# Kernel optimization log

Measured on AMD Instinct MI355X. Metric: run time of the kernel, lower is better.

The kernel has to match this reference:

```python
import jax, jax.numpy as jnp
import numpy as np
from functools import partial

H = 512
V = 32000


def setup_inputs() -> dict:
    key = jax.random.key(0)
    ks = jax.random.split(key, 16)
    B, Td, Te = 16, 64, 64
    s = 0.02
    inp = {
        'input_seqs': jax.random.normal(ks[0], (B, Td, H), jnp.float32),
        'input_lengths': jax.random.randint(ks[1], (B,), 1, Td + 1, jnp.int32),
        'encoder_outputs': jax.random.normal(ks[2], (B, Te, H), jnp.float32),
        'encoder_length': jax.random.randint(ks[3], (B,), 1, Te + 1, jnp.int32),
        # GRU (1 layer, batch_first): PyTorch layout W_ih (3H,H), W_hh (3H,H)
        'W_ih': jax.random.normal(ks[4], (3 * H, H), jnp.float32) * s,
        'W_hh': jax.random.normal(ks[5], (3 * H, H), jnp.float32) * s,
        'b_ih': jnp.zeros((3 * H,), jnp.float32),
        'b_hh': jnp.zeros((3 * H,), jnp.float32),
        # Attn: W: Linear(2H -> H), v: Linear(H -> 1)
        'W_attn': jax.random.normal(ks[6], (H, 2 * H), jnp.float32) * s,
        'b_attn': jnp.zeros((H,), jnp.float32),
        'v_w': jax.random.normal(ks[7], (H,), jnp.float32) * s,
        'v_b': jnp.zeros((), jnp.float32),
        # dense: Linear(2H -> H), output: Linear(H -> V)
        'W_dense': jax.random.normal(ks[8], (H, 2 * H), jnp.float32) * s,
        'b_dense': jnp.zeros((H,), jnp.float32),
        'W_out': jax.random.normal(ks[9], (V, H), jnp.float32) * s,
        'b_out': jnp.zeros((V,), jnp.float32),
    }
    return inp


def gru_forward(x, lengths, W_ih, W_hh, b_ih, b_hh):
    # Emulates pack_padded_sequence + GRU + pad_packed_sequence:
    # hidden state frozen past each sequence's length, outputs zero there.
    B, T, Hd = x.shape
    x_proj = jnp.einsum('bth,gh->btg', x, W_ih) + b_ih  # (B,T,3H)

    def step(h, inp):
        xp, t = inp  # xp: (B,3H)
        hp = h @ W_hh.T + b_hh
        xr, xz, xn = jnp.split(xp, 3, axis=-1)
        hr, hz, hn = jnp.split(hp, 3, axis=-1)
        r = jax.nn.sigmoid(xr + hr)
        z = jax.nn.sigmoid(xz + hz)
        n = jnp.tanh(xn + r * hn)
        h_new = (1.0 - z) * n + z * h
        valid = (t < lengths)[:, None]
        h_keep = jnp.where(valid, h_new, h)
        y = jnp.where(valid, h_new, 0.0)
        return h_keep, y

    h0 = jnp.zeros((B, Hd), x.dtype)
    h_last, ys = jax.lax.scan(step, h0, (x_proj.swapaxes(0, 1), jnp.arange(T)))
    return ys.swapaxes(0, 1), h_last  # (B,T,H), (B,H)


def attn_forward(enc, dec, enc_len, dec_len, W_attn, b_attn, v_w, v_b):
    B, Te, Hd = enc.shape
    Td = dec.shape[1]
    e_mask = (jnp.arange(Te) < enc_len[:, None])  # (B,Te)
    d_mask = (jnp.arange(Td) < dec_len[:, None])  # (B,Td)
    mask = (d_mask[:, :, None] & e_mask[:, None, :]).astype(enc.dtype)  # (B,Td,Te)
    # split W on the concat axis: cat(enc,dec) @ W.T = enc@We.T + dec@Wd.T
    We, Wd = W_attn[:, :Hd], W_attn[:, Hd:]
    enc_p = jnp.einsum('beh,gh->beg', enc, We)  # (B,Te,H)
    dec_p = jnp.einsum('bdh,gh->bdg', dec, Wd)  # (B,Td,H)
    m4 = mask[..., None]
    # masked-then-projected, matching enc_outputs*mask / dec_outputs*mask in torch
    score = jnp.tanh(enc_p[:, None, :, :] * m4 + dec_p[:, :, None, :] * m4 + b_attn)  # (B,Td,Te,H)
    energy = jnp.einsum('bdeh,h->bde', score, v_w) + v_b  # (B,Td,Te)
    a = jax.nn.softmax(energy, axis=2)  # softmax over ALL Te incl. masked (faithful)
    a_m = a * mask
    s = a_m.sum(axis=2)
    s = jnp.where(s == 0, 1.0, s)
    attention = a_m / s[:, :, None]  # (B,Td,Te)
    # attention is already zero where mask==0, so enc*mask == plain enc here
    context = jnp.einsum('bde,beh->bdh', attention, enc)
    return context  # dropout is identity at eval


def reference(input_seqs, input_lengths, encoder_outputs, encoder_length,
              W_ih, W_hh, b_ih, b_hh, W_attn, b_attn, v_w, v_b,
              W_dense, b_dense, W_out, b_out):
    dec_out, h_last = gru_forward(input_seqs, input_lengths, W_ih, W_hh, b_ih, b_hh)
    context = attn_forward(encoder_outputs, dec_out, encoder_length, input_lengths,
                           W_attn, b_attn, v_w, v_b)
    outputs = jnp.concatenate((dec_out, context), axis=2)  # (B,Td,2H)
    dense = jnp.tanh(jnp.einsum('bdg,hg->bdh', outputs, W_dense) + b_dense)
    logits = jnp.einsum('bdh,vh->bdv', dense, W_out) + b_out  # (B,Td,V)
    return logits, h_last[None]  # hidden: (n_layers=1, B, H)
```

## Files before the change

### kernel.cpp

```cpp
#include <hip/hip_runtime.h>
#include <stdint.h>


#define Hdim 512
#define Vdim 32000
#define Bdim 16
#define Tdim 64
#define BT   1024
#define GANG_BLOCKS 16
#define CVT_BLOCKS 64

typedef __attribute__((ext_vector_type(8))) short bf16x8;
typedef __attribute__((ext_vector_type(4))) float f32x4;

static __device__ __forceinline__ unsigned short f2bf(float f) {
    unsigned u = __float_as_uint(f);
    u = u + 0x7FFFu + ((u >> 16) & 1u);
    return (unsigned short)(u >> 16);
}
static __device__ __forceinline__ float bf2f(unsigned short h) {
    return __uint_as_float((unsigned)h << 16);
}
static __device__ __forceinline__ float fast_tanh(float x) {
    return 2.f / (1.f + __expf(-2.f * x)) - 1.f;
}


#define U_ZERO 8320
#define U_INP  131072
#define U_WIH  196608
#define U_WAT  131072
#define U_WDE  131072
#define U_ENC  131072
#define U_SPLIT (U_INP + U_WIH + U_WAT + U_WDE + U_ENC)
#define U_TOT  (U_ZERO + U_SPLIT)

__global__ __launch_bounds__(256) void preproc_kernel(
    const float* __restrict__ input_seqs,
    const float* __restrict__ W_ih,
    const float* __restrict__ W_attn,
    const float* __restrict__ W_dense,
    const float* __restrict__ enc,
    float* __restrict__ zero_base,
    unsigned short* __restrict__ inp_h, unsigned short* __restrict__ inp_l,
    unsigned short* __restrict__ Wih_h, unsigned short* __restrict__ Wih_l,
    unsigned short* __restrict__ Wat_h, unsigned short* __restrict__ Wat_l,
    unsigned short* __restrict__ Wde_h, unsigned short* __restrict__ Wde_l,
    unsigned short* __restrict__ enc_h, unsigned short* __restrict__ enc_l)
{
    int u = blockIdx.x * 256 + threadIdx.x;
    const int stride = gridDim.x * 256;
    for (; u < U_TOT; u += stride) {
        int r = u;
        if (r < U_ZERO) {
            float4 z; z.x = 0.f; z.y = 0.f; z.z = 0.f; z.w = 0.f;
            *(float4*)(zero_base + r * 4) = z;
            continue;
        }
        r -= U_ZERO;
        const float* src; unsigned short* hi; unsigned short* lo;
        if (r < U_INP) { src = input_seqs; hi = inp_h; lo = inp_l; }
        else { r -= U_INP;
            if (r < U_WIH) { src = W_ih; hi = Wih_h; lo = Wih_l; }
            else { r -= U_WIH;
                if (r < U_WAT) { src = W_attn; hi = Wat_h; lo = Wat_l; }
                else { r -= U_WAT;
                    if (r < U_WDE) { src = W_dense; hi = Wde_h; lo = Wde_l; }
                    else { r -= U_WDE; src = enc; hi = enc_h; lo = enc_l; }
                }
            }
        }
        int i = r * 4;
        float4 v = *(const float4*)(src + i);
        float f[4] = {v.x, v.y, v.z, v.w};
        unsigned short h[4], l[4];
#pragma unroll
        for (int k = 0; k < 4; ++k) {
            h[k] = f2bf(f[k]);
            l[k] = f2bf(f[k] - bf2f(h[k]));
        }
        *(uint2*)(hi + i) = *(const uint2*)h;
        *(uint2*)(lo + i) = *(const uint2*)l;
    }
}


struct GemmSmem {
    unsigned short AsH[128 * 40];
    unsigned short AsL[128 * 40];
    unsigned short BsH[128 * 40];
    unsigned short BsL[128 * 40];
};

static __device__ __forceinline__ void gemm_tile(
    GemmSmem& S, int m0, int n0,
    const unsigned short* __restrict__ Ah, const unsigned short* __restrict__ Al, int lda,
    const unsigned short* __restrict__ Bh, const unsigned short* __restrict__ Bl, int ldb,
    const float* __restrict__ bias,
    float* __restrict__ C, unsigned short* __restrict__ Cb, int ldc,
    int K, int act)
{
    const int tid = threadIdx.x;
    const int wave = tid >> 6, lane = tid & 63;
    const int wm = (wave >> 1) * 64, wn = (wave & 1) * 64;
    const int lrow = lane & 15, lk = (lane >> 4) * 8;

    f32x4 acc[4][4];
#pragma unroll
    for (int i = 0; i < 4; ++i)
#pragma unroll
        for (int j = 0; j < 4; ++j) acc[i][j] = (f32x4){0.f, 0.f, 0.f, 0.f};

    for (int k0 = 0; k0 < K; k0 += 32) {
#pragma unroll
        for (int i = 0; i < 2; ++i) {
            int idx = tid + i * 256;
            int rr = idx >> 2, kq = (idx & 3) * 8;
            size_t ao = (size_t)(m0 + rr) * lda + k0 + kq;
            size_t bo = (size_t)(n0 + rr) * ldb + k0 + kq;
            *(uint4*)(&S.AsH[rr * 40 + kq]) = *(const uint4*)(Ah + ao);
            *(uint4*)(&S.AsL[rr * 40 + kq]) = *(const uint4*)(Al + ao);
            *(uint4*)(&S.BsH[rr * 40 + kq]) = *(const uint4*)(Bh + bo);
            *(uint4*)(&S.BsL[rr * 40 + kq]) = *(const uint4*)(Bl + bo);
        }
        __syncthreads();
        bf16x8 ah[4], al[4], bh[4], bl[4];
#pragma unroll
        for (int i = 0; i < 4; ++i) {
            ah[i] = *(const bf16x8*)(&S.AsH[(wm + i * 16 + lrow) * 40 + lk]);
            al[i] = *(const bf16x8*)(&S.AsL[(wm + i * 16 + lrow) * 40 + lk]);
        }
#pragma unroll
        for (int j = 0; j < 4; ++j) {
            bh[j] = *(const bf16x8*)(&S.BsH[(wn + j * 16 + lrow) * 40 + lk]);
            bl[j] = *(const bf16x8*)(&S.BsL[(wn + j * 16 + lrow) * 40 + lk]);
        }
#pragma unroll
        for (int i = 0; i < 4; ++i)
#pragma unroll
            for (int j = 0; j < 4; ++j) {
                acc[i][j] = __builtin_amdgcn_mfma_f32_16x16x32_bf16(ah[i], bh[j], acc[i][j], 0, 0, 0);
                acc[i][j] = __builtin_amdgcn_mfma_f32_16x16x32_bf16(ah[i], bl[j], acc[i][j], 0, 0, 0);
                acc[i][j] = __builtin_amdgcn_mfma_f32_16x16x32_bf16(al[i], bh[j], acc[i][j], 0, 0, 0);
            }
        __syncthreads();
    }

    const int crow = m0 + wm + ((lane >> 4) * 4);
    const int ccol = n0 + wn + (lane & 15);
#pragma unroll
    for (int i = 0; i < 4; ++i) {
#pragma unroll
        for (int j = 0; j < 4; ++j) {
            int col = ccol + j * 16;
            float bv = bias[col];
#pragma unroll
            for (int rr = 0; rr < 4; ++rr) {
                int row = crow + i * 16 + rr;
                float v = acc[i][j][rr] + bv;
                if (act == 1) v = fast_tanh(v);
                if (Cb) Cb[(size_t)row * ldc + col] = f2bf(v);
                else    C [(size_t)row * ldc + col] = v;
            }
        }
    }
}

__global__ __launch_bounds__(256) void gemm_split(
    const unsigned short* __restrict__ Ah, const unsigned short* __restrict__ Al, int lda,
    const unsigned short* __restrict__ Bh, const unsigned short* __restrict__ Bl, int ldb,
    const float* __restrict__ bias,
    float* __restrict__ C, unsigned short* __restrict__ Cb, int ldc,
    int K, int act)
{
    __shared__ GemmSmem S;
    gemm_tile(S, blockIdx.y * 128, blockIdx.x * 128,
              Ah, Al, lda, Bh, Bl, ldb, bias, C, Cb, ldc, K, act);
}

__global__ __launch_bounds__(256) void gemm_split_dual(
    const unsigned short* __restrict__ A0h, const unsigned short* __restrict__ A0l,
    const unsigned short* __restrict__ B0h, const unsigned short* __restrict__ B0l,
    const float* __restrict__ bias0, float* __restrict__ C0,
    const unsigned short* __restrict__ A1h, const unsigned short* __restrict__ A1l,
    const unsigned short* __restrict__ B1h, const unsigned short* __restrict__ B1l,
    const float* __restrict__ bias1, float* __restrict__ C1)
{
    __shared__ GemmSmem S;
    const int bid = blockIdx.x;
    if (bid < 96) {
        gemm_tile(S, (bid / 12) * 128, (bid % 12) * 128,
                  A0h, A0l, Hdim, B0h, B0l, Hdim, bias0, C0, nullptr, 1536, Hdim, 0);
    } else {
        int r = bid - 96;
        gemm_tile(S, (r / 4) * 128, (r % 4) * 128,
                  A1h, A1l, Hdim, B1h, B1l, 1024, bias1, C1, nullptr, Hdim, Hdim, 0);
    }
}


__global__ __launch_bounds__(512) void gru_fused(
    const float* __restrict__ xp,
    const float* __restrict__ Whh,
    const float* __restrict__ bhh,
    const int*   __restrict__ lengths,
    unsigned long long* __restrict__ hslots,
    unsigned short* __restrict__ cath,
    unsigned short* __restrict__ catl,
    float* __restrict__ h_last,
    const float* __restrict__ Wout_f,
    unsigned short* __restrict__ Wout_bf)
{
    const int bid  = blockIdx.x;
    const int tid  = threadIdx.x;

    if (bid >= Bdim * GANG_BLOCKS) {
        int u = (bid - Bdim * GANG_BLOCKS) * 512 + tid;
        const int STR = CVT_BLOCKS * 512;
        for (; u < (Vdim * Hdim) / 4; u += STR) {
            float4 v = *(const float4*)(Wout_f + (size_t)u * 4);
            unsigned short h[4] = {f2bf(v.x), f2bf(v.y), f2bf(v.z), f2bf(v.w)};
            *(uint2*)(Wout_bf + (size_t)u * 4) = *(const uint2*)h;
        }
        return;
    }

    const int b    = bid >> 4;
    const int blk  = bid & 15;
    const int wave = tid >> 6, lane = tid & 63;
    const int j0 = blk * 32 + wave * 4;
    const int k0 = lane * 8;

    __shared__ float hl[2][512];
    __shared__ unsigned short yh_buf[64][32];
    __shared__ unsigned short yl_buf[64][32];

    float w[12][8];
#pragma unroll
    for (int g = 0; g < 3; ++g)
#pragma unroll
        for (int jj = 0; jj < 4; ++jj) {
            const float* src = Whh + (size_t)(g * 512 + j0 + jj) * Hdim + k0;
            float4 a = *(const float4*)src;
            float4 bq = *(const float4*)(src + 4);
            int r = g * 4 + jj;
            w[r][0] = a.x;  w[r][1] = a.y;  w[r][2] = a.z;  w[r][3] = a.w;
            w[r][4] = bq.x; w[r][5] = bq.y; w[r][6] = bq.z; w[r][7] = bq.w;
        }

    const int j = j0 + (lane & 3);
    float bh_r = 0.f, bh_z = 0.f, bh_n = 0.f;
    if (lane < 4) {
        bh_r = bhh[j]; bh_z = bhh[512 + j]; bh_n = bhh[1024 + j];
    }
    const int len_b = lengths[b];
    float hprev = 0.f;

    const size_t PSTR = (size_t)Bdim * Hdim;
    unsigned long long* gslot = hslots + (size_t)b * Hdim;
    const float* xbase = xp + (size_t)b * Tdim * 1536;

    for (int t = 0; t < Tdim; ++t) {
        const int par = t & 1;

        float xr = 0.f, xz = 0.f, xn = 0.f;
        if (lane < 4) {
            const float* xrow = xbase + (size_t)t * 1536;
            xr = xrow[j]; xz = xrow[512 + j]; xn = xrow[1024 + j];
        }

        if (wave == 0) {
            const unsigned long long* sl = gslot + (size_t)par * PSTR + k0;
            unsigned long long v[8];
            bool ok;
            do {
#pragma unroll
                for (int q = 0; q < 8; ++q)
                    v[q] = __hip_atomic_load(sl + q, __ATOMIC_RELAXED,
                                             __HIP_MEMORY_SCOPE_AGENT);
                ok = true;
#pragma unroll
                for (int q = 0; q < 8; ++q)
                    ok = ok && ((unsigned)(v[q] >> 32) == (unsigned)t);
            } while (!ok);
#pragma unroll
            for (int q = 0; q < 8; ++q)
                hl[par][q * 64 + lane] = __uint_as_float((unsigned)v[q]);
        }
        __syncthreads();

        float hv[8];
#pragma unroll
        for (int q = 0; q < 8; ++q) hv[q] = hl[par][q * 64 + lane];

        float p[12];
#pragma unroll
        for (int r = 0; r < 12; ++r) {
            float s = 0.f;
#pragma unroll
            for (int k = 0; k < 8; ++k) s += w[r][k] * hv[k];
            p[r] = s;
        }

#pragma unroll
        for (int off = 1; off < 64; off <<= 1)
#pragma unroll
            for (int r = 0; r < 12; ++r)
                p[r] += __shfl_xor(p[r], off);

        if (lane < 4) {
            const int jj = lane;
            float hr = p[jj]     + bh_r;
            float hz = p[4 + jj] + bh_z;
            float hn = p[8 + jj] + bh_n;
            float rg = 1.f / (1.f + __expf(-(xr + hr)));
            float zg = 1.f / (1.f + __expf(-(xz + hz)));
            float ng = fast_tanh(xn + rg * hn);
            float hnew = (1.f - zg) * ng + zg * hprev;
            bool valid = t < len_b;
            float hkeep = valid ? hnew : hprev;
            hprev = hkeep;
            if (t < Tdim - 1) {
                unsigned long long pv =
                    ((unsigned long long)(unsigned)(t + 1) << 32) |
                    (unsigned long long)__float_as_uint(hkeep);
                __hip_atomic_store(gslot + (size_t)((t + 1) & 1) * PSTR + j, pv,
                                   __ATOMIC_RELAXED, __HIP_MEMORY_SCOPE_AGENT);
            } else {
                h_last[b * Hdim + j] = hkeep;
            }
            float y = valid ? hnew : 0.f;
            unsigned short yh = f2bf(y);
            yh_buf[t][wave * 4 + jj] = yh;
            yl_buf[t][wave * 4 + jj] = f2bf(y - bf2f(yh));
        }
    }

    __syncthreads();
    for (int idx = tid; idx < 64 * 16; idx += 512) {
        int t = idx >> 4, c = (idx & 15) * 2;
        size_t off = (size_t)(b * Tdim + t) * 1024 + blk * 32 + c;
        *(unsigned*)(cath + off) = *(const unsigned*)(&yh_buf[t][c]);
        *(unsigned*)(catl + off) = *(const unsigned*)(&yl_buf[t][c]);
    }
}


__global__ __launch_bounds__(256) void attn_kernel(
    const float* __restrict__ encp,
    const float* __restrict__ decp,
    const float* __restrict__ enc,
    const float* __restrict__ battn,
    const float* __restrict__ vw,
    const float* __restrict__ vb,
    const int* __restrict__ enc_len,
    const int* __restrict__ dec_len,
    unsigned short* __restrict__ cath,
    unsigned short* __restrict__ catl)
{
    const int blk = blockIdx.x;
    const int b = blk >> 6, d = blk & 63;
    const int tid = threadIdx.x;
    const size_t obase = (size_t)(b * Tdim + d) * 1024 + 512;

    if (d >= dec_len[b]) {
        for (int h = tid; h < Hdim; h += 256) { cath[obase + h] = 0; catl[obase + h] = 0; }
        return;
    }
    const int Tv = enc_len[b];

    __shared__ float dpb[512];
    __shared__ float vwl[512];
    __shared__ float part[64][4];
    __shared__ float a_lds[64];

    if (tid < 128) {
        const float4* dp4 = (const float4*)(decp + (size_t)(b * Tdim + d) * Hdim);
        float4 dv = dp4[tid];
        float4 bb = ((const float4*)battn)[tid];
        float4 r; r.x = dv.x + bb.x; r.y = dv.y + bb.y;
        r.z = dv.z + bb.z; r.w = dv.w + bb.w;
        ((float4*)dpb)[tid] = r;
        ((float4*)vwl)[tid] = ((const float4*)vw)[tid];
    }
    __syncthreads();

    const int e = tid >> 2, p = tid & 3;
    float s = 0.f;
    if (e < Tv) {
        const float4* ep4 = (const float4*)(encp + (size_t)(b * Tdim + e) * Hdim);
        const int q0 = p * 32;
        for (int q = q0; q < q0 + 32; ++q) {
            float4 ev = ep4[q];
            s += vwl[q * 4 + 0] * fast_tanh(ev.x + dpb[q * 4 + 0]);
            s += vwl[q * 4 + 1] * fast_tanh(ev.y + dpb[q * 4 + 1]);
            s += vwl[q * 4 + 2] * fast_tanh(ev.z + dpb[q * 4 + 2]);
            s += vwl[q * 4 + 3] * fast_tanh(ev.w + dpb[q * 4 + 3]);
        }
    }
    part[e][p] = s;
    __syncthreads();

    if (tid < 64) {
        const int e2 = tid;
        float en = (e2 < Tv) ? (part[e2][0] + part[e2][1] + part[e2][2] + part[e2][3] + vb[0]) : -1e30f;
        float m = en;
#pragma unroll
        for (int off = 32; off; off >>= 1) m = fmaxf(m, __shfl_xor(m, off));
        float ex = (e2 < Tv) ? __expf(en - m) : 0.f;
        float sum = ex;
#pragma unroll
        for (int off = 32; off; off >>= 1) sum += __shfl_xor(sum, off);
        a_lds[e2] = ex / sum;
    }
    __syncthreads();

    const int h = tid * 2;
    float c0 = 0.f, c1 = 0.f;
    for (int e3 = 0; e3 < Tv; ++e3) {
        float a = a_lds[e3];
        float2 ev = *(const float2*)(enc + (size_t)(b * Tdim + e3) * Hdim + h);
        c0 += a * ev.x; c1 += a * ev.y;
    }
    unsigned short h0 = f2bf(c0), h1 = f2bf(c1);
    cath[obase + h]     = h0;  catl[obase + h]     = f2bf(c0 - bf2f(h0));
    cath[obase + h + 1] = h1;  catl[obase + h + 1] = f2bf(c1 - bf2f(h1));
}


__global__ __launch_bounds__(512) void gemm_logits(
    const unsigned short* __restrict__ A,
    const unsigned short* __restrict__ B,
    const float* __restrict__ bias,
    float* __restrict__ C)
{
    const int K = Hdim;
    __shared__ unsigned short As[256 * 40];
    __shared__ unsigned short Bs[128 * 40];
    const int tid = threadIdx.x;
    const int m0 = blockIdx.y * 256, n0 = blockIdx.x * 128;
    const int wave = tid >> 6, lane = tid & 63;
    const int wm = (wave >> 1) * 64, wn = (wave & 1) * 64;
    const int lrow = lane & 15, lk = (lane >> 4) * 8;

    f32x4 acc[4][4];
#pragma unroll
    for (int i = 0; i < 4; ++i)
#pragma unroll
        for (int j = 0; j < 4; ++j) acc[i][j] = (f32x4){0.f, 0.f, 0.f, 0.f};

    for (int k0 = 0; k0 < K; k0 += 32) {
#pragma unroll
        for (int i = 0; i < 2; ++i) {
            int idx = tid + i * 512;
            int rr = idx >> 2, kq = (idx & 3) * 8;
            *(uint4*)(&As[rr * 40 + kq]) = *(const uint4*)(A + (size_t)(m0 + rr) * K + k0 + kq);
        }
        {
            int rr = tid >> 2, kq = (tid & 3) * 8;
            *(uint4*)(&Bs[rr * 40 + kq]) = *(const uint4*)(B + (size_t)(n0 + rr) * K + k0 + kq);
        }
        __syncthreads();
        bf16x8 af[4], bf[4];
#pragma unroll
        for (int i = 0; i < 4; ++i) af[i] = *(const bf16x8*)(&As[(wm + i * 16 + lrow) * 40 + lk]);
#pragma unroll
        for (int j = 0; j < 4; ++j) bf[j] = *(const bf16x8*)(&Bs[(wn + j * 16 + lrow) * 40 + lk]);
#pragma unroll
        for (int i = 0; i < 4; ++i)
#pragma unroll
            for (int j = 0; j < 4; ++j)
                acc[i][j] = __builtin_amdgcn_mfma_f32_16x16x32_bf16(af[i], bf[j], acc[i][j], 0, 0, 0);
        __syncthreads();
    }

    const int crow = m0 + wm + ((lane >> 4) * 4);
    const int ccol = n0 + wn + (lane & 15);
#pragma unroll
    for (int i = 0; i < 4; ++i) {
#pragma unroll
        for (int j = 0; j < 4; ++j) {
            int col = ccol + j * 16;
            float bv = bias[col];
#pragma unroll
            for (int rr = 0; rr < 4; ++rr) {
                int row = crow + i * 16 + rr;
                C[(size_t)row * Vdim + col] = acc[i][j][rr] + bv;
            }
        }
    }
}


extern "C" void kernel_launch(void* const* d_in, const int* in_sizes, int n_in,
                              void* d_out, int out_size, void* d_ws, size_t ws_size,
                              hipStream_t stream) {
    (void)in_sizes; (void)n_in; (void)out_size; (void)ws_size;

    const float* input_seqs  = (const float*)d_in[0];
    const int*   input_len   = (const int*)  d_in[1];
    const float* enc_out     = (const float*)d_in[2];
    const int*   enc_len     = (const int*)  d_in[3];
    const float* W_ih        = (const float*)d_in[4];
    const float* W_hh        = (const float*)d_in[5];
    const float* b_ih        = (const float*)d_in[6];
    const float* b_hh        = (const float*)d_in[7];
    const float* W_attn      = (const float*)d_in[8];
    const float* b_attn      = (const float*)d_in[9];
    const float* v_w         = (const float*)d_in[10];
    const float* v_b         = (const float*)d_in[11];
    const float* W_dense     = (const float*)d_in[12];
    const float* b_dense     = (const float*)d_in[13];
    const float* W_out       = (const float*)d_in[14];
    const float* b_out       = (const float*)d_in[15];

    float* logits = (float*)d_out;
    float* h_last = (float*)d_out + (size_t)BT * Vdim;

    float* ws    = (float*)d_ws;
    float* xp    = ws;
    float* encp  = xp   + 1572864;
    float* decp  = encp + 524288;
    unsigned long long* hslots = (unsigned long long*)(decp + 524288);
    float* zbias = (float*)(hslots + 16384);
    unsigned short* U0 = (unsigned short*)(zbias + 512);
    unsigned short* inp_h   = U0;
    unsigned short* inp_l   = U0 + 524288;
    unsigned short* Wih_h   = U0 + 1048576;
    unsigned short* Wih_l   = U0 + 1835008;
    unsigned short* Wattn_h = U0 + 2621440;
    unsigned short* Wattn_l = U0 + 3145728;
    unsigned short* Wden_h  = U0 + 3670016;
    unsigned short* Wden_l  = U0 + 4194304;
    unsigned short* enc_h   = U0 + 4718592;
    unsigned short* enc_l   = U0 + 5242880;
    unsigned short* Wout_bf = U0 + 5767168;
    unsigned short* cath = U0;
    unsigned short* catl = U0 + 1048576;
    unsigned short* dense_bf = (unsigned short*)encp;

    preproc_kernel<<<1024, 256, 0, stream>>>(
        input_seqs, W_ih, W_attn, W_dense, enc_out,
        (float*)hslots,
        inp_h, inp_l, Wih_h, Wih_l, Wattn_h, Wattn_l,
        Wden_h, Wden_l, enc_h, enc_l);

    gemm_split_dual<<<128, 256, 0, stream>>>(
        inp_h, inp_l, Wih_h, Wih_l, b_ih, xp,
        enc_h, enc_l, Wattn_h, Wattn_l, zbias, encp);

    gru_fused<<<Bdim * GANG_BLOCKS + CVT_BLOCKS, 512, 0, stream>>>(
        xp, W_hh, b_hh, input_len, hslots, cath, catl, h_last,
        W_out, Wout_bf);

    gemm_split<<<dim3(Hdim / 128, BT / 128), 256, 0, stream>>>(
        cath, catl, 1024, Wattn_h + 512, Wattn_l + 512, 1024, zbias, decp, nullptr, Hdim, Hdim, 0);

    attn_kernel<<<BT, 256, 0, stream>>>(encp, decp, enc_out, b_attn, v_w, v_b,
                                        enc_len, input_len, cath, catl);

    gemm_split<<<dim3(Hdim / 128, BT / 128), 256, 0, stream>>>(
        cath, catl, 1024, Wden_h, Wden_l, 1024, b_dense, nullptr, dense_bf, Hdim, 1024, 1);

    gemm_logits<<<dim3(Vdim / 128, BT / 256), 512, 0, stream>>>(
        dense_bf, Wout_bf, b_out, logits);
}
```

Before: 699.6 us.

## Fuse bf16 hi/lo splitting into GEMM tile loads and move W_out conversion earlier

Drops the separate preprocessing pass that split fp32 inputs and weights into bf16 hi/lo arrays. The GEMM tile loader now reads fp32 directly and splits it while staging into shared memory. The W_out fp32-to-bf16 conversion moves out of the GRU launch into extra blocks of the first dual GEMM, so the GRU gang runs alone. This removes a full write and read of the split copies, but the B operand is re-split by every tile that uses it, and the GEMMs read twice as many bytes per element.

```diff
diff --git a/kernel.cpp b/kernel.cpp
--- a/kernel.cpp
+++ b/kernel.cpp
@@ -8,7 +8,6 @@
 #define Tdim 64
 #define BT   1024
 #define GANG_BLOCKS 16
-#define CVT_BLOCKS 64
 
 typedef __attribute__((ext_vector_type(8))) short bf16x8;
 typedef __attribute__((ext_vector_type(4))) float f32x4;
@@ -26,61 +25,11 @@
 }
 
 
-#define U_ZERO 8320
-#define U_INP  131072
-#define U_WIH  196608
-#define U_WAT  131072
-#define U_WDE  131072
-#define U_ENC  131072
-#define U_SPLIT (U_INP + U_WIH + U_WAT + U_WDE + U_ENC)
-#define U_TOT  (U_ZERO + U_SPLIT)
-
-__global__ __launch_bounds__(256) void preproc_kernel(
-    const float* __restrict__ input_seqs,
-    const float* __restrict__ W_ih,
-    const float* __restrict__ W_attn,
-    const float* __restrict__ W_dense,
-    const float* __restrict__ enc,
-    float* __restrict__ zero_base,
-    unsigned short* __restrict__ inp_h, unsigned short* __restrict__ inp_l,
-    unsigned short* __restrict__ Wih_h, unsigned short* __restrict__ Wih_l,
-    unsigned short* __restrict__ Wat_h, unsigned short* __restrict__ Wat_l,
-    unsigned short* __restrict__ Wde_h, unsigned short* __restrict__ Wde_l,
-    unsigned short* __restrict__ enc_h, unsigned short* __restrict__ enc_l)
-{
+__global__ __launch_bounds__(256) void zero_kernel(float* __restrict__ p) {
     int u = blockIdx.x * 256 + threadIdx.x;
-    const int stride = gridDim.x * 256;
-    for (; u < U_TOT; u += stride) {
-        int r = u;
-        if (r < U_ZERO) {
-            float4 z; z.x = 0.f; z.y = 0.f; z.z = 0.f; z.w = 0.f;
-            *(float4*)(zero_base + r * 4) = z;
-            continue;
-        }
-        r -= U_ZERO;
-        const float* src; unsigned short* hi; unsigned short* lo;
-        if (r < U_INP) { src = input_seqs; hi = inp_h; lo = inp_l; }
-        else { r -= U_INP;
-            if (r < U_WIH) { src = W_ih; hi = Wih_h; lo = Wih_l; }
-            else { r -= U_WIH;
-                if (r < U_WAT) { src = W_attn; hi = Wat_h; lo = Wat_l; }
-                else { r -= U_WAT;
-                    if (r < U_WDE) { src = W_dense; hi = Wde_h; lo = Wde_l; }
-                    else { r -= U_WDE; src = enc; hi = enc_h; lo = enc_l; }
-                }
-            }
-        }
-        int i = r * 4;
-        float4 v = *(const float4*)(src + i);
-        float f[4] = {v.x, v.y, v.z, v.w};
-        unsigned short h[4], l[4];
-#pragma unroll
-        for (int k = 0; k < 4; ++k) {
-            h[k] = f2bf(f[k]);
-            l[k] = f2bf(f[k] - bf2f(h[k]));
-        }
-        *(uint2*)(hi + i) = *(const uint2*)h;
-        *(uint2*)(lo + i) = *(const uint2*)l;
+    if (u < 8320) {
+        float4 z; z.x = 0.f; z.y = 0.f; z.z = 0.f; z.w = 0.f;
+        *(float4*)(p + u * 4) = z;
     }
 }
 
@@ -92,10 +41,28 @@
     unsigned short BsL[128 * 40];
 };
 
+static __device__ __forceinline__ void split8(const float* __restrict__ src,
+                                              unsigned short* __restrict__ dh,
+                                              unsigned short* __restrict__ dl) {
+    float4 v0 = *(const float4*)src;
+    float4 v1 = *(const float4*)(src + 4);
+    float f[8] = {v0.x, v0.y, v0.z, v0.w, v1.x, v1.y, v1.z, v1.w};
+    unsigned short h[8], l[8];
+#pragma unroll
+    for (int k = 0; k < 8; ++k) {
+        h[k] = f2bf(f[k]);
+        l[k] = f2bf(f[k] - bf2f(h[k]));
+    }
+    *(uint4*)dh = *(const uint4*)h;
+    *(uint4*)dl = *(const uint4*)l;
+}
+
 static __device__ __forceinline__ void gemm_tile(
     GemmSmem& S, int m0, int n0,
-    const unsigned short* __restrict__ Ah, const unsigned short* __restrict__ Al, int lda,
-    const unsigned short* __restrict__ Bh, const unsigned short* __restrict__ Bl, int ldb,
+    const unsigned short* __restrict__ Ah, const unsigned short* __restrict__ Al,
+    const float* __restrict__ Af, int lda,
+    const unsigned short* __restrict__ Bh, const unsigned short* __restrict__ Bl,
+    const float* __restrict__ Bf, int ldb,
     const float* __restrict__ bias,
     float* __restrict__ C, unsigned short* __restrict__ Cb, int ldc,
     int K, int act)
@@ -116,12 +83,22 @@
         for (int i = 0; i < 2; ++i) {
             int idx = tid + i * 256;
             int rr = idx >> 2, kq = (idx & 3) * 8;
-            size_t ao = (size_t)(m0 + rr) * lda + k0 + kq;
-            size_t bo = (size_t)(n0 + rr) * ldb + k0 + kq;
-            *(uint4*)(&S.AsH[rr * 40 + kq]) = *(const uint4*)(Ah + ao);
-            *(uint4*)(&S.AsL[rr * 40 + kq]) = *(const uint4*)(Al + ao);
-            *(uint4*)(&S.BsH[rr * 40 + kq]) = *(const uint4*)(Bh + bo);
-            *(uint4*)(&S.BsL[rr * 40 + kq]) = *(const uint4*)(Bl + bo);
+            if (Af) {
+                split8(Af + (size_t)(m0 + rr) * lda + k0 + kq,
+                       &S.AsH[rr * 40 + kq], &S.AsL[rr * 40 + kq]);
+            } else {
+                size_t ao = (size_t)(m0 + rr) * lda + k0 + kq;
+                *(uint4*)(&S.AsH[rr * 40 + kq]) = *(const uint4*)(Ah + ao);
+                *(uint4*)(&S.AsL[rr * 40 + kq]) = *(const uint4*)(Al + ao);
+            }
+            if (Bf) {
+                split8(Bf + (size_t)(n0 + rr) * ldb + k0 + kq,
+                       &S.BsH[rr * 40 + kq], &S.BsL[rr * 40 + kq]);
+            } else {
+                size_t bo = (size_t)(n0 + rr) * ldb + k0 + kq;
+                *(uint4*)(&S.BsH[rr * 40 + kq]) = *(const uint4*)(Bh + bo);
+                *(uint4*)(&S.BsL[rr * 40 + kq]) = *(const uint4*)(Bl + bo);
+            }
         }
         __syncthreads();
         bf16x8 ah[4], al[4], bh[4], bl[4];
@@ -168,38 +145,55 @@
 
 __global__ __launch_bounds__(256) void gemm_split(
     const unsigned short* __restrict__ Ah, const unsigned short* __restrict__ Al, int lda,
-    const unsigned short* __restrict__ Bh, const unsigned short* __restrict__ Bl, int ldb,
+    const float* __restrict__ Bf, int ldb,
     const float* __restrict__ bias,
     float* __restrict__ C, unsigned short* __restrict__ Cb, int ldc,
     int K, int act)
 {
     __shared__ GemmSmem S;
     gemm_tile(S, blockIdx.y * 128, blockIdx.x * 128,
-              Ah, Al, lda, Bh, Bl, ldb, bias, C, Cb, ldc, K, act);
-}
-
-__global__ __launch_bounds__(256) void gemm_split_dual(
-    const unsigned short* __restrict__ A0h, const unsigned short* __restrict__ A0l,
-    const unsigned short* __restrict__ B0h, const unsigned short* __restrict__ B0l,
+              Ah, Al, nullptr, lda, nullptr, nullptr, Bf, ldb,
+              bias, C, Cb, ldc, K, act);
+}
+
+__global__ __launch_bounds__(256) void gemm_dual_cvt(
+    const float* __restrict__ input_seqs,
+    const float* __restrict__ W_ih,
     const float* __restrict__ bias0, float* __restrict__ C0,
-    const unsigned short* __restrict__ A1h, const unsigned short* __restrict__ A1l,
-    const unsigned short* __restrict__ B1h, const unsigned short* __restrict__ B1l,
-    const float* __restrict__ bias1, float* __restrict__ C1)
+    const float* __restrict__ enc,
+    const float* __restrict__ W_attn,
+    const float* __restrict__ bias1, float* __restrict__ C1,
+    const float* __restrict__ Wout_f,
+    unsigned short* __restrict__ Wout_bf)
 {
+    const int bid = blockIdx.x;
+    if (bid >= 128) {
+        int u = (bid - 128) * 256 + threadIdx.x;
+        const int STR = 128 * 256;
+        for (; u < (Vdim * Hdim) / 4; u += STR) {
+            float4 v = *(const float4*)(Wout_f + (size_t)u * 4);
+            unsigned short h[4] = {f2bf(v.x), f2bf(v.y), f2bf(v.z), f2bf(v.w)};
+            *(uint2*)(Wout_bf + (size_t)u * 4) = *(const uint2*)h;
+        }
+        return;
+    }
     __shared__ GemmSmem S;
-    const int bid = blockIdx.x;
     if (bid < 96) {
         gemm_tile(S, (bid / 12) * 128, (bid % 12) * 128,
-                  A0h, A0l, Hdim, B0h, B0l, Hdim, bias0, C0, nullptr, 1536, Hdim, 0);
+                  nullptr, nullptr, input_seqs, Hdim,
+                  nullptr, nullptr, W_ih, Hdim,
+                  bias0, C0, nullptr, 1536, Hdim, 0);
     } else {
         int r = bid - 96;
         gemm_tile(S, (r / 4) * 128, (r % 4) * 128,
-                  A1h, A1l, Hdim, B1h, B1l, 1024, bias1, C1, nullptr, Hdim, Hdim, 0);
-    }
-}
-
-
-__global__ __launch_bounds__(512) void gru_fused(
+                  nullptr, nullptr, enc, Hdim,
+                  nullptr, nullptr, W_attn, 1024,
+                  bias1, C1, nullptr, Hdim, Hdim, 0);
+    }
+}
+
+
+__global__ __launch_bounds__(512) void gru_persistent(
     const float* __restrict__ xp,
     const float* __restrict__ Whh,
     const float* __restrict__ bhh,
@@ -207,26 +201,12 @@
     unsigned long long* __restrict__ hslots,
     unsigned short* __restrict__ cath,
     unsigned short* __restrict__ catl,
-    float* __restrict__ h_last,
-    const float* __restrict__ Wout_f,
-    unsigned short* __restrict__ Wout_bf)
+    float* __restrict__ h_last)
 {
     const int bid  = blockIdx.x;
-    const int tid  = threadIdx.x;
-
-    if (bid >= Bdim * GANG_BLOCKS) {
-        int u = (bid - Bdim * GANG_BLOCKS) * 512 + tid;
-        const int STR = CVT_BLOCKS * 512;
-        for (; u < (Vdim * Hdim) / 4; u += STR) {
-            float4 v = *(const float4*)(Wout_f + (size_t)u * 4);
-            unsigned short h[4] = {f2bf(v.x), f2bf(v.y), f2bf(v.z), f2bf(v.w)};
-            *(uint2*)(Wout_bf + (size_t)u * 4) = *(const uint2*)h;
-        }
-        return;
-    }
-
     const int b    = bid >> 4;
     const int blk  = bid & 15;
+    const int tid  = threadIdx.x;
     const int wave = tid >> 6, lane = tid & 63;
     const int j0 = blk * 32 + wave * 4;
     const int k0 = lane * 8;
@@ -524,43 +504,29 @@
     unsigned long long* hslots = (unsigned long long*)(decp + 524288);
     float* zbias = (float*)(hslots + 16384);
     unsigned short* U0 = (unsigned short*)(zbias + 512);
-    unsigned short* inp_h   = U0;
-    unsigned short* inp_l   = U0 + 524288;
-    unsigned short* Wih_h   = U0 + 1048576;
-    unsigned short* Wih_l   = U0 + 1835008;
-    unsigned short* Wattn_h = U0 + 2621440;
-    unsigned short* Wattn_l = U0 + 3145728;
-    unsigned short* Wden_h  = U0 + 3670016;
-    unsigned short* Wden_l  = U0 + 4194304;
-    unsigned short* enc_h   = U0 + 4718592;
-    unsigned short* enc_l   = U0 + 5242880;
-    unsigned short* Wout_bf = U0 + 5767168;
-    unsigned short* cath = U0;
-    unsigned short* catl = U0 + 1048576;
+    unsigned short* cath    = U0;
+    unsigned short* catl    = U0 + 1048576;
+    unsigned short* Wout_bf = U0 + 2097152;
     unsigned short* dense_bf = (unsigned short*)encp;
 
-    preproc_kernel<<<1024, 256, 0, stream>>>(
-        input_seqs, W_ih, W_attn, W_dense, enc_out,
-        (float*)hslots,
-        inp_h, inp_l, Wih_h, Wih_l, Wattn_h, Wattn_l,
-        Wden_h, Wden_l, enc_h, enc_l);
-
-    gemm_split_dual<<<128, 256, 0, stream>>>(
-        inp_h, inp_l, Wih_h, Wih_l, b_ih, xp,
-        enc_h, enc_l, Wattn_h, Wattn_l, zbias, encp);
-
-    gru_fused<<<Bdim * GANG_BLOCKS + CVT_BLOCKS, 512, 0, stream>>>(
-        xp, W_hh, b_hh, input_len, hslots, cath, catl, h_last,
+    zero_kernel<<<33, 256, 0, stream>>>((float*)hslots);
+
+    gemm_dual_cvt<<<256, 256, 0, stream>>>(
+        input_seqs, W_ih, b_ih, xp,
+        enc_out, W_attn, zbias, encp,
         W_out, Wout_bf);
 
+    gru_persistent<<<Bdim * GANG_BLOCKS, 512, 0, stream>>>(
+        xp, W_hh, b_hh, input_len, hslots, cath, catl, h_last);
+
     gemm_split<<<dim3(Hdim / 128, BT / 128), 256, 0, stream>>>(
-        cath, catl, 1024, Wattn_h + 512, Wattn_l + 512, 1024, zbias, decp, nullptr, Hdim, Hdim, 0);
+        cath, catl, 1024, W_attn + 512, 1024, zbias, decp, nullptr, Hdim, Hdim, 0);
 
     attn_kernel<<<BT, 256, 0, stream>>>(encp, decp, enc_out, b_attn, v_w, v_b,
                                         enc_len, input_len, cath, catl);
 
     gemm_split<<<dim3(Hdim / 128, BT / 128), 256, 0, stream>>>(
-        cath, catl, 1024, Wden_h, Wden_l, 1024, b_dense, nullptr, dense_bf, Hdim, 1024, 1);
+        cath, catl, 1024, W_dense, 1024, b_dense, nullptr, dense_bf, Hdim, 1024, 1);
 
     gemm_logits<<<dim3(Vdim / 128, BT / 256), 512, 0, stream>>>(
         dense_bf, Wout_bf, b_out, logits);
```

Result: slower. 721.0 us (+3.1%).

## Move W_out bf16 conversion from GRU kernel into decoder-projection GEMM launch

Applied to the files above, without the earlier changes.

The fp32-to-bf16 conversion of W_out used to run in 64 extra blocks alongside the persistent GRU kernel. It now runs in 224 extra blocks of a new kernel that also computes the decoder attention projection GEMM (32 tiles). The GRU kernel becomes a pure persistent recurrence with 256 blocks, so the conversion no longer competes with the latency-bound recurrence for memory bandwidth or CUs. The cost is that the conversion is now serialized after the GRU instead of overlapping with it, though with more blocks working on it.

```diff
diff --git a/kernel.cpp b/kernel.cpp
--- a/kernel.cpp
+++ b/kernel.cpp
@@ -8,7 +8,6 @@
 #define Tdim 64
 #define BT   1024
 #define GANG_BLOCKS 16
-#define CVT_BLOCKS 64
 
 typedef __attribute__((ext_vector_type(8))) short bf16x8;
 typedef __attribute__((ext_vector_type(4))) float f32x4;
@@ -198,8 +197,37 @@
     }
 }
 
-
-__global__ __launch_bounds__(512) void gru_fused(
+__global__ __launch_bounds__(256) void gemm_decp_cvt(
+    const unsigned short* __restrict__ Ah, const unsigned short* __restrict__ Al,
+    const unsigned short* __restrict__ Bh, const unsigned short* __restrict__ Bl,
+    const float* __restrict__ bias,
+    float* __restrict__ C,
+    const float* __restrict__ Wout_f,
+    unsigned short* __restrict__ Wout_bf)
+{
+    const int bid = blockIdx.x;
+    if (bid >= 32) {
+        const int NG = (Vdim * Hdim) / 16;
+        int g = (bid - 32) * 256 + threadIdx.x;
+        const int stride = 224 * 256;
+        for (; g < NG; g += stride) {
+#pragma unroll
+            for (int c = 0; c < 4; ++c) {
+                size_t u = (size_t)g * 4 + c;
+                float4 v = *(const float4*)(Wout_f + u * 4);
+                unsigned short h[4] = {f2bf(v.x), f2bf(v.y), f2bf(v.z), f2bf(v.w)};
+                *(uint2*)(Wout_bf + u * 4) = *(const uint2*)h;
+            }
+        }
+        return;
+    }
+    __shared__ GemmSmem S;
+    gemm_tile(S, (bid >> 2) * 128, (bid & 3) * 128,
+              Ah, Al, 1024, Bh, Bl, 1024, bias, C, nullptr, Hdim, Hdim, 0);
+}
+
+
+__global__ __launch_bounds__(512) void gru_persistent(
     const float* __restrict__ xp,
     const float* __restrict__ Whh,
     const float* __restrict__ bhh,
@@ -207,26 +235,12 @@
     unsigned long long* __restrict__ hslots,
     unsigned short* __restrict__ cath,
     unsigned short* __restrict__ catl,
-    float* __restrict__ h_last,
-    const float* __restrict__ Wout_f,
-    unsigned short* __restrict__ Wout_bf)
+    float* __restrict__ h_last)
 {
     const int bid  = blockIdx.x;
-    const int tid  = threadIdx.x;
-
-    if (bid >= Bdim * GANG_BLOCKS) {
-        int u = (bid - Bdim * GANG_BLOCKS) * 512 + tid;
-        const int STR = CVT_BLOCKS * 512;
-        for (; u < (Vdim * Hdim) / 4; u += STR) {
-            float4 v = *(const float4*)(Wout_f + (size_t)u * 4);
-            unsigned short h[4] = {f2bf(v.x), f2bf(v.y), f2bf(v.z), f2bf(v.w)};
-            *(uint2*)(Wout_bf + (size_t)u * 4) = *(const uint2*)h;
-        }
-        return;
-    }
-
     const int b    = bid >> 4;
     const int blk  = bid & 15;
+    const int tid  = threadIdx.x;
     const int wave = tid >> 6, lane = tid & 63;
     const int j0 = blk * 32 + wave * 4;
     const int k0 = lane * 8;
@@ -549,12 +563,12 @@
         inp_h, inp_l, Wih_h, Wih_l, b_ih, xp,
         enc_h, enc_l, Wattn_h, Wattn_l, zbias, encp);
 
-    gru_fused<<<Bdim * GANG_BLOCKS + CVT_BLOCKS, 512, 0, stream>>>(
-        xp, W_hh, b_hh, input_len, hslots, cath, catl, h_last,
+    gru_persistent<<<Bdim * GANG_BLOCKS, 512, 0, stream>>>(
+        xp, W_hh, b_hh, input_len, hslots, cath, catl, h_last);
+
+    gemm_decp_cvt<<<256, 256, 0, stream>>>(
+        cath, catl, Wattn_h + 512, Wattn_l + 512, zbias, decp,
         W_out, Wout_bf);
-
-    gemm_split<<<dim3(Hdim / 128, BT / 128), 256, 0, stream>>>(
-        cath, catl, 1024, Wattn_h + 512, Wattn_l + 512, 1024, zbias, decp, nullptr, Hdim, Hdim, 0);
 
     attn_kernel<<<BT, 256, 0, stream>>>(encp, decp, enc_out, b_attn, v_w, v_b,
                                         enc_len, input_len, cath, catl);
```

New measurement: 659.6 us. -5.7%, faster.
